# Kernel tuning notes

Measured on AMD Instinct MI355X. Metric: run time of the kernel, lower is better.

Reference implementation:

```python
import jax, jax.numpy as jnp
import numpy as np
import math

B, M, H, K, SPAN = 8, 1024, 512, 8, 1024
D = H // K
MK = M + SPAN


def _skew(X, pad_value):
    # shift every row one step to the right: [N, M, L] -> [N, M, M+L]
    N, m, L = X.shape
    X = jnp.pad(X, ((0, 0), (0, 0), (0, m + 1)), constant_values=pad_value)
    X = X.reshape(N, -1)[:, :-m]
    return X.reshape(N, m, m + L)


def _unskew(X):
    # reverse of _skew: [N, M, M+L] -> [N, M, L]
    N, m, Lk = X.shape
    L = Lk - m
    X = jnp.pad(X.reshape(N, -1), ((0, 0), (0, m)))
    return X.reshape(N, m, Lk + 1)[:, :, :L]


def setup_inputs() -> dict:
    key0 = jax.random.key(0)
    ks = jax.random.split(key0, 8)
    w_scale = 1.0 / math.sqrt(H)
    return {
        "query": jax.random.normal(ks[0], (B, M, H), jnp.float32),
        "key": jax.random.normal(ks[1], (B, MK, H), jnp.float32),
        "value": jax.random.normal(ks[2], (B, MK, H), jnp.float32),
        "pos_encoding": jax.random.normal(ks[3], (D, SPAN), jnp.float32) * w_scale,
        "Wq": jax.random.normal(ks[4], (H, H), jnp.float32) * w_scale,
        "Wk": jax.random.normal(ks[5], (H, H), jnp.float32) * w_scale,
        "Wv": jax.random.normal(ks[6], (H, H), jnp.float32) * w_scale,
        "Wo": jax.random.normal(ks[7], (H, H), jnp.float32) * w_scale,
    }


def _heads(x, W):
    # project then split heads: [B, T, H] -> [B*K, T, D]
    x = x @ W
    Bx, T, _ = x.shape
    x = x.reshape(Bx, T, K, D).transpose(0, 2, 1, 3)
    return x.reshape(Bx * K, T, D)


def reference(query, key, value, pos_encoding, Wq, Wk, Wv, Wo):
    q = _heads(query, Wq)      # [B*K, M, D]
    k = _heads(key, Wk)        # [B*K, MK, D]
    v = _heads(value, Wv)      # [B*K, MK, D]

    attn_ctx = jnp.einsum("nmd,nld->nml", q, k)   # [B*K, M, MK]
    attn_ctx = _unskew(attn_ctx)                    # [B*K, M, SPAN]
    attn_pos = jnp.einsum("nmd,ds->nms", q, pos_encoding)  # [B*K, M, SPAN]
    attn = jax.nn.softmax((attn_ctx + attn_pos) / math.sqrt(D), axis=-1)

    attn_sk = _skew(attn, 0.0)                      # [B*K, M, MK]
    out = jnp.einsum("nml,nld->nmd", attn_sk, v)   # [B*K, M, D]
    out = out.reshape(B, K, M, D).transpose(0, 2, 1, 3).reshape(B, M, H)
    return out @ Wo
```

## Files before the change

kernel.cpp:

```cpp
#include <hip/hip_runtime.h>
#include <stdint.h>

#define Bq 8
#define Mq 1024
#define Hq 512
#define NHq 8
#define Dq 64
#define SPANq 1024
#define MKq 2048
#define PR2 168

typedef __bf16 bf16x8 __attribute__((ext_vector_type(8)));
typedef _Float16 f16x8 __attribute__((ext_vector_type(8)));
typedef float f32x4 __attribute__((ext_vector_type(4)));
typedef unsigned short ushort8 __attribute__((ext_vector_type(8)));
typedef unsigned int uint2v __attribute__((ext_vector_type(2)));

static __device__ __forceinline__ unsigned short f2bf(float f) {
  union { float f; unsigned u; } x; x.f = f;
  unsigned r = x.u + 0x7FFFu + ((x.u >> 16) & 1u);
  return (unsigned short)(r >> 16);
}

static __device__ __forceinline__ unsigned pk_f16(float a, float b) {
  return __builtin_bit_cast(unsigned, __builtin_amdgcn_cvt_pkrtz(a, b));
}

static __device__ __forceinline__ f32x4 mfma_bf16(bf16x8 a, bf16x8 b, f32x4 c) {
  return __builtin_amdgcn_mfma_f32_16x16x32_bf16(a, b, c, 0, 0, 0);
}
static __device__ __forceinline__ f32x4 mfma_f16(f16x8 a, f16x8 b, f32x4 c) {
  return __builtin_amdgcn_mfma_f32_16x16x32_f16(a, b, c, 0, 0, 0);
}

static __device__ __forceinline__ void async_ld16(const void* g, void* l) {
  __builtin_amdgcn_global_load_lds(
      (const __attribute__((address_space(1))) void*)g,
      (__attribute__((address_space(3))) void*)l, 16, 0, 0);
}

__global__ __launch_bounds__(256) void conv_bf16(
    const float* __restrict__ q, const float* __restrict__ k,
    const float* __restrict__ v, unsigned short* __restrict__ qo,
    unsigned short* __restrict__ ko, unsigned short* __restrict__ vo) {
  const int z = blockIdx.y;
  const float* src = (z == 0) ? q : (z == 1) ? k : v;
  unsigned short* dst = (z == 0) ? qo : (z == 1) ? ko : vo;
  const int n = (z == 0) ? (Bq * Mq * Hq) : (Bq * MKq * Hq);
  const int idx = (blockIdx.x * 256 + threadIdx.x) * 8;
  if (idx >= n) return;
  const f32x4 f0 = *(const f32x4*)(src + idx);
  const f32x4 f1 = *(const f32x4*)(src + idx + 4);
  ushort8 h;
  h[0] = f2bf(f0[0]); h[1] = f2bf(f0[1]); h[2] = f2bf(f0[2]); h[3] = f2bf(f0[3]);
  h[4] = f2bf(f1[0]); h[5] = f2bf(f1[1]); h[6] = f2bf(f1[2]); h[7] = f2bf(f1[3]);
  *(ushort8*)(dst + idx) = h;
}

__global__ __launch_bounds__(256) void prep_transpose(
    const float* __restrict__ Wq, const float* __restrict__ Wk,
    const float* __restrict__ Wv, const float* __restrict__ Wo,
    const float* __restrict__ pos,
    unsigned short* __restrict__ WTq, unsigned short* __restrict__ WTk,
    unsigned short* __restrict__ WTv, unsigned short* __restrict__ WTo,
    unsigned short* __restrict__ posT) {
  __shared__ float tile[64][65];
  const int bid = blockIdx.x;
  const float* src; unsigned short* dst;
  int src_stride, dst_stride, i0, o0;
  if (bid < 256) {
    const int w = bid >> 6, t = bid & 63;
    src = (w == 0) ? Wq : (w == 1) ? Wk : (w == 2) ? Wv : Wo;
    dst = (w == 0) ? WTq : (w == 1) ? WTk : (w == 2) ? WTv : WTo;
    src_stride = Hq; dst_stride = Hq;
    i0 = (t >> 3) * 64; o0 = (t & 7) * 64;
  } else {
    const int t = bid - 256;
    src = pos; dst = posT;
    src_stride = SPANq; dst_stride = Dq;
    i0 = 0; o0 = t * 64;
  }
  const int tid = threadIdx.x;
  for (int e = tid; e < 4096; e += 256) {
    const int r = e >> 6, c = e & 63;
    tile[r][c] = src[(size_t)(i0 + r) * src_stride + o0 + c];
  }
  __syncthreads();
  for (int e = tid; e < 4096; e += 256) {
    const int r = e >> 6, c = e & 63;
    dst[(size_t)(o0 + r) * dst_stride + i0 + c] = f2bf(tile[c][r]);
  }
}

__global__ __launch_bounds__(256, 2) void gemm128(
    const unsigned short* __restrict__ Xb, const unsigned short* __restrict__ WT,
    unsigned short* __restrict__ outb, _Float16* __restrict__ outv,
    float* __restrict__ outf, int mode, int tshift) {
  __shared__ unsigned short sh[18432];
  unsigned short* As = sh;
  unsigned short* Bs = sh + 8192;
  const int tid = threadIdx.x;
  const int wave = tid >> 6, lane = tid & 63;
  const int q = lane >> 4, l16 = lane & 15;
  const int wy = wave >> 1, wx = wave & 1;
  const size_t m0 = (size_t)blockIdx.x * 128;
  const int n0 = blockIdx.y * 128;
  const int dsub = lane >> 3;
  const int dswz = (lane & 7) ^ dsub;

  f32x4 acc[4][4] = {};

  for (int k0 = 0; k0 < Hq; k0 += 64) {
    __syncthreads();
#pragma unroll
    for (int i = 0; i < 4; i++) {
      const int s = wave * 4 + i;
      const int r = s * 8 + dsub;
      async_ld16(Xb + (m0 + r) * Hq + k0 + dswz * 8, As + s * 512);
      async_ld16(WT + (size_t)(n0 + r) * Hq + k0 + dswz * 8, Bs + s * 512);
    }
    __syncthreads();
    bf16x8 af[2][4], bg[2][4];
#pragma unroll
    for (int h = 0; h < 2; h++) {
#pragma unroll
      for (int mt = 0; mt < 4; mt++) {
        const int R = wy * 64 + mt * 16 + l16;
        af[h][mt] = *(const bf16x8*)(As + R * 64 + (((h * 4 + q) ^ (l16 & 7)) * 8));
      }
#pragma unroll
      for (int nt = 0; nt < 4; nt++) {
        const int R = wx * 64 + nt * 16 + l16;
        bg[h][nt] = *(const bf16x8*)(Bs + R * 64 + (((h * 4 + q) ^ (l16 & 7)) * 8));
      }
    }
#pragma unroll
    for (int h = 0; h < 2; h++)
#pragma unroll
      for (int mt = 0; mt < 4; mt++)
#pragma unroll
        for (int nt = 0; nt < 4; nt++)
          acc[mt][nt] = mfma_bf16(af[h][mt], bg[h][nt], acc[mt][nt]);
  }

  if (mode == 2) {
    __syncthreads();
    _Float16* tr = (_Float16*)sh + wave * 4608;
#pragma unroll
    for (int nt = 0; nt < 4; nt++)
#pragma unroll
      for (int mt = 0; mt < 4; mt++)
#pragma unroll
        for (int r = 0; r < 4; r++)
          tr[(nt * 16 + l16) * 72 + mt * 16 + q * 4 + r] = (_Float16)acc[mt][nt][r];
    const int head = blockIdx.y * 2 + wx;
    const int mrow0 = (int)m0 + wy * 64;
    const int Tlen = 1 << tshift;
    const int b = mrow0 >> tshift, t0 = mrow0 & (Tlen - 1);
#pragma unroll
    for (int it = 0; it < 8; it++) {
      const int dl = it * 8 + (lane >> 3), tl = (lane & 7) * 8;
      const f16x8 v = *(const f16x8*)(tr + dl * 72 + tl);
      *(f16x8*)(outv + ((size_t)((b * 8 + head) * 64 + dl)) * Tlen + t0 + tl) = v;
    }
    return;
  }

  const int Tlen = 1 << tshift;
#pragma unroll
  for (int mt = 0; mt < 4; mt++) {
#pragma unroll
    for (int nt = 0; nt < 4; nt++) {
      const int c = n0 + wx * 64 + nt * 16 + l16;
#pragma unroll
      for (int r = 0; r < 4; r++) {
        const int m = (int)m0 + wy * 64 + mt * 16 + q * 4 + r;
        const float val = acc[mt][nt][r];
        if (mode == 3) {
          outf[(size_t)m * Hq + c] = val;
        } else {
          const int b = m >> tshift, t = m & (Tlen - 1);
          const int head = c >> 6, d = c & 63;
          outb[(((size_t)(b * 8 + head) << tshift) + t) * 64 + d] = f2bf(val);
        }
      }
    }
  }
}

__global__ __launch_bounds__(256, 2) void attn3(
    const unsigned short* __restrict__ qb, const unsigned short* __restrict__ kglob,
    const _Float16* __restrict__ vT, const unsigned short* __restrict__ posT,
    unsigned short* __restrict__ ctx) {
  __shared__ unsigned short Kt[12288];
  __shared__ unsigned short Pt[8192];
  __shared__ unsigned short Psh[4 * 16 * PR2];

  const int tid = threadIdx.x;
  const int wave = tid >> 6, lane = tid & 63;
  const int q = lane >> 4, l16 = lane & 15;
  const int n = blockIdx.y;
  const int m0 = blockIdx.x * 64;
  const int m0w = m0 + wave * 16;
  const int dsub = lane >> 3;
  const int dswz = (lane & 7) ^ dsub;

  unsigned short* row = Psh + (wave * 16 + l16) * PR2;

  const unsigned short* qbase = qb + ((size_t)n * Mq + m0w + l16) * Dq;
  const bf16x8 qf0 = *(const bf16x8*)(qbase + q * 8);
  const bf16x8 qf1 = *(const bf16x8*)(qbase + 32 + q * 8);

  const unsigned short* kbn = kglob + (size_t)n * MKq * Dq;
  const _Float16* vbn = vT + (size_t)n * Dq * MKq;

  f32x4 O[4] = {};
  float zrow = 0.f, mrow = -1e30f;

  for (int c = 0; c < 8; c++) {
    const int sbase = c * 128;
    const int jb = m0 + sbase;
    const int j00 = m0w + sbase;

    __syncthreads();
#pragma unroll
    for (int i = 0; i < 6; i++) {
      const int s = wave + 4 * i;
      const int r = s * 8 + dsub;
      async_ld16(kbn + (size_t)(jb + r) * Dq + dswz * 8, Kt + s * 512);
    }
#pragma unroll
    for (int i = 0; i < 4; i++) {
      const int s = wave + 4 * i;
      const int r = s * 8 + dsub;
      async_ld16(posT + (size_t)(sbase + r) * Dq + dswz * 8, Pt + s * 512);
    }
    __syncthreads();

#pragma unroll
    for (int t = 0; t < 8; t++) {
      const int rl = t * 16 + l16;
      const int ch = (q ^ (l16 & 7)) * 8;
      const bf16x8 p0 = *(const bf16x8*)(Pt + rl * 64 + ch);
      const bf16x8 p1 = *(const bf16x8*)(Pt + rl * 64 + (ch ^ 32));
      f32x4 b = {};
      b = mfma_bf16(p0, qf0, b);
      b = mfma_bf16(p1, qf1, b);
      const int cw = 16 + t * 16 + 4 * q + l16;
      row[cw + 0] = f2bf(b[0]);
      row[cw + 1] = f2bf(b[1]);
      row[cw + 2] = f2bf(b[2]);
      row[cw + 3] = f2bf(b[3]);
    }

    f32x4 S[9];
#pragma unroll
    for (int t = 0; t < 9; t++) {
      const int rl = wave * 16 + t * 16 + l16;
      const int ch = (q ^ (l16 & 7)) * 8;
      const bf16x8 k0 = *(const bf16x8*)(Kt + rl * 64 + ch);
      const bf16x8 k1 = *(const bf16x8*)(Kt + rl * 64 + (ch ^ 32));
      f32x4 a = {};
      a = mfma_bf16(k0, qf0, a);
      a = mfma_bf16(k1, qf1, a);
      const uint2v pv = *(const uint2v*)(row + 16 + t * 16 + 4 * q);
      a[0] += __uint_as_float(pv.x << 16);
      a[1] += __uint_as_float(pv.x & 0xffff0000u);
      a[2] += __uint_as_float(pv.y << 16);
      a[3] += __uint_as_float(pv.y & 0xffff0000u);
      S[t] = a;
    }
#pragma unroll
    for (int r = 0; r < 4; r++) {
      if (4 * q + r < l16) S[0][r] = -1e30f;
      if (4 * q + r >= l16) S[8][r] = -1e30f;
    }

    float mx = -1e30f;
#pragma unroll
    for (int t = 0; t < 9; t++)
      mx = fmaxf(mx, fmaxf(fmaxf(S[t][0], S[t][1]), fmaxf(S[t][2], S[t][3])));
    mx = fmaxf(mx, __shfl_xor(mx, 16, 64));
    mx = fmaxf(mx, __shfl_xor(mx, 32, 64));
    const float m_new = fmaxf(mrow, mx);
    const float alpha = __expf((mrow - m_new) * 0.125f);
    float zs = 0.f;
#pragma unroll
    for (int t = 0; t < 9; t++) {
#pragma unroll
      for (int r = 0; r < 4; r++) {
        const float e = __expf((S[t][r] - m_new) * 0.125f);
        S[t][r] = e; zs += e;
      }
    }
    zs += __shfl_xor(zs, 16, 64);
    zs += __shfl_xor(zs, 32, 64);
    zrow = zrow * alpha + zs;
    mrow = m_new;
#pragma unroll
    for (int dt = 0; dt < 4; dt++) O[dt] *= alpha;

#pragma unroll
    for (int t = 0; t < 9; t++) {
      *(unsigned*)(row + t * 16 + 4 * q) = pk_f16(S[t][0], S[t][1]);
      *(unsigned*)(row + t * 16 + 4 * q + 2) = pk_f16(S[t][2], S[t][3]);
    }
    *(unsigned*)(row + 144 + 4 * q) = 0u;
    *(unsigned*)(row + 144 + 4 * q + 2) = 0u;

    f16x8 Bf[5];
#pragma unroll
    for (int kt = 0; kt < 5; kt++)
      Bf[kt] = *(const f16x8*)(row + kt * 32 + q * 8);
    f16x8 Vv[5][4];
#pragma unroll
    for (int kt = 0; kt < 5; kt++) {
      int j = j00 + kt * 32 + q * 8;
      if (j > MKq - 8) j = MKq - 8;
#pragma unroll
      for (int dt = 0; dt < 4; dt++)
        Vv[kt][dt] = *(const f16x8*)(vbn + (size_t)(dt * 16 + l16) * MKq + j);
    }
#pragma unroll
    for (int kt = 0; kt < 5; kt++)
#pragma unroll
      for (int dt = 0; dt < 4; dt++)
        O[dt] = mfma_f16(Vv[kt][dt], Bf[kt], O[dt]);
  }

  const float zi = 1.f / zrow;
  unsigned short* cp = ctx + ((size_t)(n >> 3) * Mq + m0w + l16) * Hq + (n & 7) * Dq;
#pragma unroll
  for (int dt = 0; dt < 4; dt++)
#pragma unroll
    for (int r = 0; r < 4; r++)
      cp[dt * 16 + q * 4 + r] = f2bf(O[dt][r] * zi);
}

extern "C" void kernel_launch(void* const* d_in, const int* in_sizes, int n_in,
                              void* d_out, int out_size, void* d_ws, size_t ws_size,
                              hipStream_t stream) {
  const float* query = (const float*)d_in[0];
  const float* key   = (const float*)d_in[1];
  const float* value = (const float*)d_in[2];
  const float* pos   = (const float*)d_in[3];
  const float* Wq    = (const float*)d_in[4];
  const float* Wk    = (const float*)d_in[5];
  const float* Wv    = (const float*)d_in[6];
  const float* Wo    = (const float*)d_in[7];
  float* out = (float*)d_out;

  char* w = (char*)d_ws;
  unsigned short* qX   = (unsigned short*)w; w += (size_t)Bq * Mq * Hq * 2;
  unsigned short* kX   = (unsigned short*)w; w += (size_t)Bq * MKq * Hq * 2;
  unsigned short* vX   = (unsigned short*)w; w += (size_t)Bq * MKq * Hq * 2;
  unsigned short* qb   = (unsigned short*)w; w += (size_t)64 * Mq * Dq * 2;
  unsigned short* kbuf = (unsigned short*)w; w += (size_t)64 * MKq * Dq * 2;
  _Float16*       vTb  = (_Float16*)w;       w += (size_t)64 * Dq * MKq * 2;
  unsigned short* posT = (unsigned short*)w; w += (size_t)SPANq * Dq * 2;
  unsigned short* WTq  = (unsigned short*)w; w += (size_t)Hq * Hq * 2;
  unsigned short* WTk  = (unsigned short*)w; w += (size_t)Hq * Hq * 2;
  unsigned short* WTv  = (unsigned short*)w; w += (size_t)Hq * Hq * 2;
  unsigned short* WTo  = (unsigned short*)w; w += (size_t)Hq * Hq * 2;
  unsigned short* ctx  = (unsigned short*)w; w += (size_t)Bq * Mq * Hq * 2;

  prep_transpose<<<272, 256, 0, stream>>>(Wq, Wk, Wv, Wo, pos, WTq, WTk, WTv, WTo, posT);
  conv_bf16<<<dim3(4096, 3), 256, 0, stream>>>(query, key, value, qX, kX, vX);
  gemm128<<<dim3(64, 4), 256, 0, stream>>>(qX, WTq, qb, nullptr, nullptr, 0, 10);
  gemm128<<<dim3(128, 4), 256, 0, stream>>>(kX, WTk, kbuf, nullptr, nullptr, 0, 11);
  gemm128<<<dim3(128, 4), 256, 0, stream>>>(vX, WTv, nullptr, vTb, nullptr, 2, 11);
  attn3<<<dim3(16, 64), 256, 0, stream>>>(qb, kbuf, vTb, posT, ctx);
  gemm128<<<dim3(64, 4), 256, 0, stream>>>(ctx, WTo, nullptr, nullptr, out, 3, 10);
}
```

Before: 287.4 us.

## Load K and pos tiles directly from global, remap blocks for XCD locality

Removes the shared-memory staging of K and position-encoding tiles (and the two block barriers per chunk), so each wave reads its MFMA operands straight from global memory through the caches. Blocks are launched as a 1D grid and remapped so that consecutive blocks on the same XCD share a head, improving L2 reuse of K/V. Also raises wave priority around the PV MFMA loop. This trades cooperative LDS reuse for more global/L2 traffic and uncoalesced 16-byte loads, in exchange for fewer syncs and less LDS use, which may allow more occupancy.

Result: slower. 373.8 us (+30.0%).

```diff
diff --git a/kernel.cpp b/kernel.cpp
--- a/kernel.cpp
+++ b/kernel.cpp
@@ -192,18 +192,17 @@
     const unsigned short* __restrict__ qb, const unsigned short* __restrict__ kglob,
     const _Float16* __restrict__ vT, const unsigned short* __restrict__ posT,
     unsigned short* __restrict__ ctx) {
-  __shared__ unsigned short Kt[12288];
-  __shared__ unsigned short Pt[8192];
   __shared__ unsigned short Psh[4 * 16 * PR2];
 
   const int tid = threadIdx.x;
   const int wave = tid >> 6, lane = tid & 63;
   const int q = lane >> 4, l16 = lane & 15;
-  const int n = blockIdx.y;
-  const int m0 = blockIdx.x * 64;
+
+  const int bid = blockIdx.x;
+  const int orig = (bid & 7) * 128 + (bid >> 3);
+  const int n = orig >> 4;
+  const int m0 = (orig & 15) * 64;
   const int m0w = m0 + wave * 16;
-  const int dsub = lane >> 3;
-  const int dswz = (lane & 7) ^ dsub;
 
   unsigned short* row = Psh + (wave * 16 + l16) * PR2;
 
@@ -213,36 +212,21 @@
 
   const unsigned short* kbn = kglob + (size_t)n * MKq * Dq;
   const _Float16* vbn = vT + (size_t)n * Dq * MKq;
+  const unsigned short* kb0 = kbn + (size_t)(m0 + wave * 16 + l16) * Dq + q * 8;
+  const unsigned short* pb0 = posT + (size_t)l16 * Dq + q * 8;
 
   f32x4 O[4] = {};
   float zrow = 0.f, mrow = -1e30f;
 
   for (int c = 0; c < 8; c++) {
-    const int sbase = c * 128;
-    const int jb = m0 + sbase;
-    const int j00 = m0w + sbase;
-
-    __syncthreads();
-#pragma unroll
-    for (int i = 0; i < 6; i++) {
-      const int s = wave + 4 * i;
-      const int r = s * 8 + dsub;
-      async_ld16(kbn + (size_t)(jb + r) * Dq + dswz * 8, Kt + s * 512);
-    }
-#pragma unroll
-    for (int i = 0; i < 4; i++) {
-      const int s = wave + 4 * i;
-      const int r = s * 8 + dsub;
-      async_ld16(posT + (size_t)(sbase + r) * Dq + dswz * 8, Pt + s * 512);
-    }
-    __syncthreads();
+    const int j00 = m0w + c * 128;
+    const unsigned short* pc = pb0 + c * 128 * Dq;
+    const unsigned short* kc = kb0 + c * 128 * Dq;
 
 #pragma unroll
     for (int t = 0; t < 8; t++) {
-      const int rl = t * 16 + l16;
-      const int ch = (q ^ (l16 & 7)) * 8;
-      const bf16x8 p0 = *(const bf16x8*)(Pt + rl * 64 + ch);
-      const bf16x8 p1 = *(const bf16x8*)(Pt + rl * 64 + (ch ^ 32));
+      const bf16x8 p0 = *(const bf16x8*)(pc + t * 16 * Dq);
+      const bf16x8 p1 = *(const bf16x8*)(pc + t * 16 * Dq + 32);
       f32x4 b = {};
       b = mfma_bf16(p0, qf0, b);
       b = mfma_bf16(p1, qf1, b);
@@ -256,10 +240,8 @@
     f32x4 S[9];
 #pragma unroll
     for (int t = 0; t < 9; t++) {
-      const int rl = wave * 16 + t * 16 + l16;
-      const int ch = (q ^ (l16 & 7)) * 8;
-      const bf16x8 k0 = *(const bf16x8*)(Kt + rl * 64 + ch);
-      const bf16x8 k1 = *(const bf16x8*)(Kt + rl * 64 + (ch ^ 32));
+      const bf16x8 k0 = *(const bf16x8*)(kc + t * 16 * Dq);
+      const bf16x8 k1 = *(const bf16x8*)(kc + t * 16 * Dq + 32);
       f32x4 a = {};
       a = mfma_bf16(k0, qf0, a);
       a = mfma_bf16(k1, qf1, a);
@@ -321,11 +303,13 @@
       for (int dt = 0; dt < 4; dt++)
         Vv[kt][dt] = *(const f16x8*)(vbn + (size_t)(dt * 16 + l16) * MKq + j);
     }
+    __builtin_amdgcn_s_setprio(1);
 #pragma unroll
     for (int kt = 0; kt < 5; kt++)
 #pragma unroll
       for (int dt = 0; dt < 4; dt++)
         O[dt] = mfma_f16(Vv[kt][dt], Bf[kt], O[dt]);
+    __builtin_amdgcn_s_setprio(0);
   }
 
   const float zi = 1.f / zrow;
@@ -369,6 +353,6 @@
   gemm128<<<dim3(64, 4), 256, 0, stream>>>(qX, WTq, qb, nullptr, nullptr, 0, 10);
   gemm128<<<dim3(128, 4), 256, 0, stream>>>(kX, WTk, kbuf, nullptr, nullptr, 0, 11);
   gemm128<<<dim3(128, 4), 256, 0, stream>>>(vX, WTv, nullptr, vTb, nullptr, 2, 11);
-  attn3<<<dim3(16, 64), 256, 0, stream>>>(qb, kbuf, vTb, posT, ctx);
+  attn3<<<dim3(1024), 256, 0, stream>>>(qb, kbuf, vTb, posT, ctx);
   gemm128<<<dim3(64, 4), 256, 0, stream>>>(ctx, WTo, nullptr, nullptr, out, 3, 10);
 }
```

## Merge QKV projections into one launch and halve attention span chunk for occupancy

Applied to the files above, without the earlier changes.

The three separate Q/K/V projection GEMM launches become one gemm_qkv kernel that routes blocks by blockIdx.x, which removes launch gaps and tail effects between them. The attention kernel now processes the span in 16 chunks of 64 instead of 8 chunks of 128. This shrinks the K, pos and P shared buffers and the per-thread score registers, and launch bounds are raised to 4 blocks per CU. In exchange there are twice as many loop iterations, barriers and rescale steps. Overlap waste also goes up, since each chunk computes a 5-tile diagonal band for 4 useful tiles, compared with 9 for 8 before.

Measured after the change: 310.2 us. +7.9%, slower.

```diff
diff --git a/kernel.cpp b/kernel.cpp
--- a/kernel.cpp
+++ b/kernel.cpp
@@ -8,7 +8,7 @@
 #define Dq 64
 #define SPANq 1024
 #define MKq 2048
-#define PR2 168
+#define PR2 104
 
 typedef __bf16 bf16x8 __attribute__((ext_vector_type(8)));
 typedef _Float16 f16x8 __attribute__((ext_vector_type(8)));
@@ -92,19 +92,19 @@
   }
 }
 
-__global__ __launch_bounds__(256, 2) void gemm128(
+static __device__ __forceinline__ void gemm_body(
     const unsigned short* __restrict__ Xb, const unsigned short* __restrict__ WT,
     unsigned short* __restrict__ outb, _Float16* __restrict__ outv,
-    float* __restrict__ outf, int mode, int tshift) {
-  __shared__ unsigned short sh[18432];
+    float* __restrict__ outf, int mode, int tshift, int bx, int by,
+    unsigned short* sh) {
   unsigned short* As = sh;
   unsigned short* Bs = sh + 8192;
   const int tid = threadIdx.x;
   const int wave = tid >> 6, lane = tid & 63;
   const int q = lane >> 4, l16 = lane & 15;
   const int wy = wave >> 1, wx = wave & 1;
-  const size_t m0 = (size_t)blockIdx.x * 128;
-  const int n0 = blockIdx.y * 128;
+  const size_t m0 = (size_t)bx * 128;
+  const int n0 = by * 128;
   const int dsub = lane >> 3;
   const int dswz = (lane & 7) ^ dsub;
 
@@ -153,7 +153,7 @@
 #pragma unroll
         for (int r = 0; r < 4; r++)
           tr[(nt * 16 + l16) * 72 + mt * 16 + q * 4 + r] = (_Float16)acc[mt][nt][r];
-    const int head = blockIdx.y * 2 + wx;
+    const int head = by * 2 + wx;
     const int mrow0 = (int)m0 + wy * 64;
     const int Tlen = 1 << tshift;
     const int b = mrow0 >> tshift, t0 = mrow0 & (Tlen - 1);
@@ -188,12 +188,38 @@
   }
 }
 
-__global__ __launch_bounds__(256, 2) void attn3(
+__global__ __launch_bounds__(256, 2) void gemm128(
+    const unsigned short* __restrict__ Xb, const unsigned short* __restrict__ WT,
+    unsigned short* __restrict__ outb, _Float16* __restrict__ outv,
+    float* __restrict__ outf, int mode, int tshift) {
+  __shared__ unsigned short sh[18432];
+  gemm_body(Xb, WT, outb, outv, outf, mode, tshift, blockIdx.x, blockIdx.y, sh);
+}
+
+__global__ __launch_bounds__(256, 2) void gemm_qkv(
+    const unsigned short* __restrict__ qX, const unsigned short* __restrict__ kX,
+    const unsigned short* __restrict__ vX,
+    const unsigned short* __restrict__ WTq, const unsigned short* __restrict__ WTk,
+    const unsigned short* __restrict__ WTv,
+    unsigned short* __restrict__ qb, unsigned short* __restrict__ kbuf,
+    _Float16* __restrict__ vTb) {
+  __shared__ unsigned short sh[18432];
+  const int x = blockIdx.x;
+  const unsigned short* Xb; const unsigned short* WT;
+  unsigned short* outb = nullptr; _Float16* outv = nullptr;
+  int mode, tshift, bx;
+  if (x < 64)       { Xb = qX; WT = WTq; outb = qb;   mode = 0; tshift = 10; bx = x; }
+  else if (x < 192) { Xb = kX; WT = WTk; outb = kbuf; mode = 0; tshift = 11; bx = x - 64; }
+  else              { Xb = vX; WT = WTv; outv = vTb;  mode = 2; tshift = 11; bx = x - 192; }
+  gemm_body(Xb, WT, outb, outv, nullptr, mode, tshift, bx, blockIdx.y, sh);
+}
+
+__global__ __launch_bounds__(256, 4) void attn3(
     const unsigned short* __restrict__ qb, const unsigned short* __restrict__ kglob,
     const _Float16* __restrict__ vT, const unsigned short* __restrict__ posT,
     unsigned short* __restrict__ ctx) {
-  __shared__ unsigned short Kt[12288];
-  __shared__ unsigned short Pt[8192];
+  __shared__ unsigned short Kt[8192];
+  __shared__ unsigned short Pt[4096];
   __shared__ unsigned short Psh[4 * 16 * PR2];
 
   const int tid = threadIdx.x;
@@ -217,20 +243,20 @@
   f32x4 O[4] = {};
   float zrow = 0.f, mrow = -1e30f;
 
-  for (int c = 0; c < 8; c++) {
-    const int sbase = c * 128;
+  for (int c = 0; c < 16; c++) {
+    const int sbase = c * 64;
     const int jb = m0 + sbase;
     const int j00 = m0w + sbase;
 
     __syncthreads();
 #pragma unroll
-    for (int i = 0; i < 6; i++) {
+    for (int i = 0; i < 4; i++) {
       const int s = wave + 4 * i;
       const int r = s * 8 + dsub;
       async_ld16(kbn + (size_t)(jb + r) * Dq + dswz * 8, Kt + s * 512);
     }
 #pragma unroll
-    for (int i = 0; i < 4; i++) {
+    for (int i = 0; i < 2; i++) {
       const int s = wave + 4 * i;
       const int r = s * 8 + dsub;
       async_ld16(posT + (size_t)(sbase + r) * Dq + dswz * 8, Pt + s * 512);
@@ -238,7 +264,7 @@
     __syncthreads();
 
 #pragma unroll
-    for (int t = 0; t < 8; t++) {
+    for (int t = 0; t < 4; t++) {
       const int rl = t * 16 + l16;
       const int ch = (q ^ (l16 & 7)) * 8;
       const bf16x8 p0 = *(const bf16x8*)(Pt + rl * 64 + ch);
@@ -253,9 +279,9 @@
       row[cw + 3] = f2bf(b[3]);
     }
 
-    f32x4 S[9];
-#pragma unroll
-    for (int t = 0; t < 9; t++) {
+    f32x4 S[5];
+#pragma unroll
+    for (int t = 0; t < 5; t++) {
       const int rl = wave * 16 + t * 16 + l16;
       const int ch = (q ^ (l16 & 7)) * 8;
       const bf16x8 k0 = *(const bf16x8*)(Kt + rl * 64 + ch);
@@ -273,12 +299,12 @@
 #pragma unroll
     for (int r = 0; r < 4; r++) {
       if (4 * q + r < l16) S[0][r] = -1e30f;
-      if (4 * q + r >= l16) S[8][r] = -1e30f;
+      if (4 * q + r >= l16) S[4][r] = -1e30f;
     }
 
     float mx = -1e30f;
 #pragma unroll
-    for (int t = 0; t < 9; t++)
+    for (int t = 0; t < 5; t++)
       mx = fmaxf(mx, fmaxf(fmaxf(S[t][0], S[t][1]), fmaxf(S[t][2], S[t][3])));
     mx = fmaxf(mx, __shfl_xor(mx, 16, 64));
     mx = fmaxf(mx, __shfl_xor(mx, 32, 64));
@@ -286,7 +312,7 @@
     const float alpha = __expf((mrow - m_new) * 0.125f);
     float zs = 0.f;
 #pragma unroll
-    for (int t = 0; t < 9; t++) {
+    for (int t = 0; t < 5; t++) {
 #pragma unroll
       for (int r = 0; r < 4; r++) {
         const float e = __expf((S[t][r] - m_new) * 0.125f);
@@ -301,20 +327,20 @@
     for (int dt = 0; dt < 4; dt++) O[dt] *= alpha;
 
 #pragma unroll
-    for (int t = 0; t < 9; t++) {
+    for (int t = 0; t < 5; t++) {
       *(unsigned*)(row + t * 16 + 4 * q) = pk_f16(S[t][0], S[t][1]);
       *(unsigned*)(row + t * 16 + 4 * q + 2) = pk_f16(S[t][2], S[t][3]);
     }
-    *(unsigned*)(row + 144 + 4 * q) = 0u;
-    *(unsigned*)(row + 144 + 4 * q + 2) = 0u;
-
-    f16x8 Bf[5];
-#pragma unroll
-    for (int kt = 0; kt < 5; kt++)
+    *(unsigned*)(row + 80 + 4 * q) = 0u;
+    *(unsigned*)(row + 80 + 4 * q + 2) = 0u;
+
+    f16x8 Bf[3];
+#pragma unroll
+    for (int kt = 0; kt < 3; kt++)
       Bf[kt] = *(const f16x8*)(row + kt * 32 + q * 8);
-    f16x8 Vv[5][4];
-#pragma unroll
-    for (int kt = 0; kt < 5; kt++) {
+    f16x8 Vv[3][4];
+#pragma unroll
+    for (int kt = 0; kt < 3; kt++) {
       int j = j00 + kt * 32 + q * 8;
       if (j > MKq - 8) j = MKq - 8;
 #pragma unroll
@@ -322,7 +348,7 @@
         Vv[kt][dt] = *(const f16x8*)(vbn + (size_t)(dt * 16 + l16) * MKq + j);
     }
 #pragma unroll
-    for (int kt = 0; kt < 5; kt++)
+    for (int kt = 0; kt < 3; kt++)
 #pragma unroll
       for (int dt = 0; dt < 4; dt++)
         O[dt] = mfma_f16(Vv[kt][dt], Bf[kt], O[dt]);
@@ -366,9 +392,7 @@
 
   prep_transpose<<<272, 256, 0, stream>>>(Wq, Wk, Wv, Wo, pos, WTq, WTk, WTv, WTo, posT);
   conv_bf16<<<dim3(4096, 3), 256, 0, stream>>>(query, key, value, qX, kX, vX);
-  gemm128<<<dim3(64, 4), 256, 0, stream>>>(qX, WTq, qb, nullptr, nullptr, 0, 10);
-  gemm128<<<dim3(128, 4), 256, 0, stream>>>(kX, WTk, kbuf, nullptr, nullptr, 0, 11);
-  gemm128<<<dim3(128, 4), 256, 0, stream>>>(vX, WTv, nullptr, vTb, nullptr, 2, 11);
+  gemm_qkv<<<dim3(320, 4), 256, 0, stream>>>(qX, kX, vX, WTq, WTk, WTv, qb, kbuf, vTb);
   attn3<<<dim3(16, 64), 256, 0, stream>>>(qb, kbuf, vTb, posT, ctx);
   gemm128<<<dim3(64, 4), 256, 0, stream>>>(ctx, WTo, nullptr, nullptr, out, 3, 10);
 }
```

## Fuse fp32-to-bf16 input conversion into a single batched QKV projection GEMM

Applied to the files above, without the earlier changes.

Removes the separate conversion kernel and its bf16 staging buffers. The new QKV GEMM loads fp32 activations straight into LDS and converts them to bf16 with packed convert instructions while building the MFMA operands. The three projection launches are merged into one grid that dispatches Q, K or V by block index. This cuts a full read-write pass over the inputs and two launches, but doubles the LDS footprint for the A tile and adds conversion ALU work inside the GEMM loop.

Measured after the change: 276.8 us. 1.04x faster.

```diff
diff --git a/kernel.cpp b/kernel.cpp
--- a/kernel.cpp
+++ b/kernel.cpp
@@ -15,6 +15,7 @@
 typedef float f32x4 __attribute__((ext_vector_type(4)));
 typedef unsigned short ushort8 __attribute__((ext_vector_type(8)));
 typedef unsigned int uint2v __attribute__((ext_vector_type(2)));
+typedef unsigned int uint4v __attribute__((ext_vector_type(4)));
 
 static __device__ __forceinline__ unsigned short f2bf(float f) {
   union { float f; unsigned u; } x; x.f = f;
@@ -26,6 +27,12 @@
   return __builtin_bit_cast(unsigned, __builtin_amdgcn_cvt_pkrtz(a, b));
 }
 
+static __device__ __forceinline__ unsigned pk_bf16(float a, float b) {
+  unsigned r;
+  asm("v_cvt_pk_bf16_f32 %0, %1, %2" : "=v"(r) : "v"(a), "v"(b));
+  return r;
+}
+
 static __device__ __forceinline__ f32x4 mfma_bf16(bf16x8 a, bf16x8 b, f32x4 c) {
   return __builtin_amdgcn_mfma_f32_16x16x32_bf16(a, b, c, 0, 0, 0);
 }
@@ -37,24 +44,6 @@
   __builtin_amdgcn_global_load_lds(
       (const __attribute__((address_space(1))) void*)g,
       (__attribute__((address_space(3))) void*)l, 16, 0, 0);
-}
-
-__global__ __launch_bounds__(256) void conv_bf16(
-    const float* __restrict__ q, const float* __restrict__ k,
-    const float* __restrict__ v, unsigned short* __restrict__ qo,
-    unsigned short* __restrict__ ko, unsigned short* __restrict__ vo) {
-  const int z = blockIdx.y;
-  const float* src = (z == 0) ? q : (z == 1) ? k : v;
-  unsigned short* dst = (z == 0) ? qo : (z == 1) ? ko : vo;
-  const int n = (z == 0) ? (Bq * Mq * Hq) : (Bq * MKq * Hq);
-  const int idx = (blockIdx.x * 256 + threadIdx.x) * 8;
-  if (idx >= n) return;
-  const f32x4 f0 = *(const f32x4*)(src + idx);
-  const f32x4 f1 = *(const f32x4*)(src + idx + 4);
-  ushort8 h;
-  h[0] = f2bf(f0[0]); h[1] = f2bf(f0[1]); h[2] = f2bf(f0[2]); h[3] = f2bf(f0[3]);
-  h[4] = f2bf(f1[0]); h[5] = f2bf(f1[1]); h[6] = f2bf(f1[2]); h[7] = f2bf(f1[3]);
-  *(ushort8*)(dst + idx) = h;
 }
 
 __global__ __launch_bounds__(256) void prep_transpose(
@@ -143,29 +132,6 @@
           acc[mt][nt] = mfma_bf16(af[h][mt], bg[h][nt], acc[mt][nt]);
   }
 
-  if (mode == 2) {
-    __syncthreads();
-    _Float16* tr = (_Float16*)sh + wave * 4608;
-#pragma unroll
-    for (int nt = 0; nt < 4; nt++)
-#pragma unroll
-      for (int mt = 0; mt < 4; mt++)
-#pragma unroll
-        for (int r = 0; r < 4; r++)
-          tr[(nt * 16 + l16) * 72 + mt * 16 + q * 4 + r] = (_Float16)acc[mt][nt][r];
-    const int head = blockIdx.y * 2 + wx;
-    const int mrow0 = (int)m0 + wy * 64;
-    const int Tlen = 1 << tshift;
-    const int b = mrow0 >> tshift, t0 = mrow0 & (Tlen - 1);
-#pragma unroll
-    for (int it = 0; it < 8; it++) {
-      const int dl = it * 8 + (lane >> 3), tl = (lane & 7) * 8;
-      const f16x8 v = *(const f16x8*)(tr + dl * 72 + tl);
-      *(f16x8*)(outv + ((size_t)((b * 8 + head) * 64 + dl)) * Tlen + t0 + tl) = v;
-    }
-    return;
-  }
-
   const int Tlen = 1 << tshift;
 #pragma unroll
   for (int mt = 0; mt < 4; mt++) {
@@ -183,6 +149,127 @@
           const int head = c >> 6, d = c & 63;
           outb[(((size_t)(b * 8 + head) << tshift) + t) * 64 + d] = f2bf(val);
         }
+      }
+    }
+  }
+}
+
+__global__ __launch_bounds__(256, 2) void gemm_qkv(
+    const float* __restrict__ qF, const float* __restrict__ kF,
+    const float* __restrict__ vF,
+    const unsigned short* __restrict__ WTq, const unsigned short* __restrict__ WTk,
+    const unsigned short* __restrict__ WTv,
+    unsigned short* __restrict__ qb, unsigned short* __restrict__ kbuf,
+    _Float16* __restrict__ vTb) {
+  __shared__ float shf[12288];
+  float* As = shf;
+  unsigned short* Bs = (unsigned short*)(shf + 8192);
+
+  const int x = blockIdx.x;
+  const float* Xf; const unsigned short* WT;
+  unsigned short* outb = nullptr; _Float16* outv = nullptr;
+  int mode, tshift, bx;
+  if (x < 64)       { Xf = qF; WT = WTq; outb = qb;   mode = 0; tshift = 10; bx = x; }
+  else if (x < 192) { Xf = kF; WT = WTk; outb = kbuf; mode = 0; tshift = 11; bx = x - 64; }
+  else              { Xf = vF; WT = WTv; outv = vTb;  mode = 2; tshift = 11; bx = x - 192; }
+
+  const int tid = threadIdx.x;
+  const int wave = tid >> 6, lane = tid & 63;
+  const int q = lane >> 4, l16 = lane & 15;
+  const int wy = wave >> 1, wx = wave & 1;
+  const size_t m0 = (size_t)bx * 128;
+  const int n0 = blockIdx.y * 128;
+  const int dsub = lane >> 3;
+  const int dswz = (lane & 7) ^ dsub;
+  const int arow = lane >> 4;
+  const int apos = lane & 15;
+
+  f32x4 acc[4][4] = {};
+
+  for (int k0 = 0; k0 < Hq; k0 += 64) {
+    __syncthreads();
+#pragma unroll
+    for (int i = 0; i < 8; i++) {
+      const int s = wave * 8 + i;
+      const int r = s * 4 + arow;
+      const int gsw = apos ^ (((s & 1) << 2) | arow);
+      async_ld16(Xf + (m0 + r) * Hq + k0 + gsw * 4, As + s * 256);
+    }
+#pragma unroll
+    for (int i = 0; i < 4; i++) {
+      const int s = wave * 4 + i;
+      const int r = s * 8 + dsub;
+      async_ld16(WT + (size_t)(n0 + r) * Hq + k0 + dswz * 8, Bs + s * 512);
+    }
+    __syncthreads();
+
+    bf16x8 af[2][4], bg[2][4];
+#pragma unroll
+    for (int h = 0; h < 2; h++) {
+#pragma unroll
+      for (int mt = 0; mt < 4; mt++) {
+        const int R = wy * 64 + mt * 16 + l16;
+        const int xr = R & 7;
+        const int c0 = h * 8 + q * 2;
+        const f32x4 a0 = *(const f32x4*)(As + R * 64 + ((c0 ^ xr) * 4));
+        const f32x4 a1 = *(const f32x4*)(As + R * 64 + (((c0 + 1) ^ xr) * 4));
+        uint4v w;
+        w[0] = pk_bf16(a0[0], a0[1]);
+        w[1] = pk_bf16(a0[2], a0[3]);
+        w[2] = pk_bf16(a1[0], a1[1]);
+        w[3] = pk_bf16(a1[2], a1[3]);
+        af[h][mt] = __builtin_bit_cast(bf16x8, w);
+      }
+#pragma unroll
+      for (int nt = 0; nt < 4; nt++) {
+        const int R = wx * 64 + nt * 16 + l16;
+        bg[h][nt] = *(const bf16x8*)(Bs + R * 64 + (((h * 4 + q) ^ (l16 & 7)) * 8));
+      }
+    }
+#pragma unroll
+    for (int h = 0; h < 2; h++)
+#pragma unroll
+      for (int mt = 0; mt < 4; mt++)
+#pragma unroll
+        for (int nt = 0; nt < 4; nt++)
+          acc[mt][nt] = mfma_bf16(af[h][mt], bg[h][nt], acc[mt][nt]);
+  }
+
+  if (mode == 2) {
+    __syncthreads();
+    _Float16* tr = (_Float16*)shf + wave * 4608;
+#pragma unroll
+    for (int nt = 0; nt < 4; nt++)
+#pragma unroll
+      for (int mt = 0; mt < 4; mt++)
+#pragma unroll
+        for (int r = 0; r < 4; r++)
+          tr[(nt * 16 + l16) * 72 + mt * 16 + q * 4 + r] = (_Float16)acc[mt][nt][r];
+    const int head = blockIdx.y * 2 + wx;
+    const int mrow0 = (int)m0 + wy * 64;
+    const int Tlen = 1 << tshift;
+    const int b = mrow0 >> tshift, t0 = mrow0 & (Tlen - 1);
+#pragma unroll
+    for (int it = 0; it < 8; it++) {
+      const int dl = it * 8 + (lane >> 3), tl = (lane & 7) * 8;
+      const f16x8 v = *(const f16x8*)(tr + dl * 72 + tl);
+      *(f16x8*)(outv + ((size_t)((b * 8 + head) * 64 + dl)) * Tlen + t0 + tl) = v;
+    }
+    return;
+  }
+
+  const int Tlen = 1 << tshift;
+#pragma unroll
+  for (int mt = 0; mt < 4; mt++) {
+#pragma unroll
+    for (int nt = 0; nt < 4; nt++) {
+      const int c = n0 + wx * 64 + nt * 16 + l16;
+#pragma unroll
+      for (int r = 0; r < 4; r++) {
+        const int m = (int)m0 + wy * 64 + mt * 16 + q * 4 + r;
+        const int b = m >> tshift, t = m & (Tlen - 1);
+        const int head = c >> 6, d = c & 63;
+        outb[(((size_t)(b * 8 + head) << tshift) + t) * 64 + d] = f2bf(acc[mt][nt][r]);
       }
     }
   }
@@ -351,9 +438,6 @@
   float* out = (float*)d_out;
 
   char* w = (char*)d_ws;
-  unsigned short* qX   = (unsigned short*)w; w += (size_t)Bq * Mq * Hq * 2;
-  unsigned short* kX   = (unsigned short*)w; w += (size_t)Bq * MKq * Hq * 2;
-  unsigned short* vX   = (unsigned short*)w; w += (size_t)Bq * MKq * Hq * 2;
   unsigned short* qb   = (unsigned short*)w; w += (size_t)64 * Mq * Dq * 2;
   unsigned short* kbuf = (unsigned short*)w; w += (size_t)64 * MKq * Dq * 2;
   _Float16*       vTb  = (_Float16*)w;       w += (size_t)64 * Dq * MKq * 2;
@@ -365,10 +449,7 @@
   unsigned short* ctx  = (unsigned short*)w; w += (size_t)Bq * Mq * Hq * 2;
 
   prep_transpose<<<272, 256, 0, stream>>>(Wq, Wk, Wv, Wo, pos, WTq, WTk, WTv, WTo, posT);
-  conv_bf16<<<dim3(4096, 3), 256, 0, stream>>>(query, key, value, qX, kX, vX);
-  gemm128<<<dim3(64, 4), 256, 0, stream>>>(qX, WTq, qb, nullptr, nullptr, 0, 10);
-  gemm128<<<dim3(128, 4), 256, 0, stream>>>(kX, WTk, kbuf, nullptr, nullptr, 0, 11);
-  gemm128<<<dim3(128, 4), 256, 0, stream>>>(vX, WTv, nullptr, vTb, nullptr, 2, 11);
+  gemm_qkv<<<dim3(320, 4), 256, 0, stream>>>(query, key, value, WTq, WTk, WTv, qb, kbuf, vTb);
   attn3<<<dim3(16, 64), 256, 0, stream>>>(qb, kbuf, vTb, posT, ctx);
   gemm128<<<dim3(64, 4), 256, 0, stream>>>(ctx, WTo, nullptr, nullptr, out, 3, 10);
 }
```
